# Optimization experiments

Hardware: AMD Instinct MI355X
Metric: run time of the kernel (lower is better)

The kernel has to match this reference:

```python
import jax, jax.numpy as jnp
import numpy as np

B, T, E = 2, 4096, 768
N_HEADS = 12
HEAD_DIM = E // N_HEADS


def setup_inputs() -> dict:
    key = jax.random.key(0)
    k1, k2, k3 = jax.random.split(key, 3)
    x = jax.random.normal(k1, (B, T, E), dtype=jnp.float32)
    W_attn = jax.random.normal(k2, (E, 3 * E), dtype=jnp.float32) * (1.0 / np.sqrt(E))
    b_attn = jnp.zeros((3 * E,), dtype=jnp.float32)
    W_proj = jax.random.normal(k3, (E, E), dtype=jnp.float32) * (1.0 / np.sqrt(E))
    b_proj = jnp.zeros((E,), dtype=jnp.float32)
    return {"x": x, "W_attn": W_attn, "b_attn": b_attn, "W_proj": W_proj, "b_proj": b_proj}


def reference(x, W_attn, b_attn, W_proj, b_proj):
    Bx, Tx, Ex = x.shape
    qkv = x @ W_attn + b_attn                      # [B,T,3E]
    q, k, v = jnp.split(qkv, 3, axis=-1)
    # [B,T,E] -> [B,H,T,D]
    def to_heads(t):
        return t.reshape(Bx, Tx, N_HEADS, HEAD_DIM).transpose(0, 2, 1, 3)
    q, k, v = to_heads(q), to_heads(k), to_heads(v)
    scale = 1.0 / np.sqrt(HEAD_DIM).astype(np.float32)
    scores = jnp.einsum('bhqd,bhkd->bhqk', q, k) * scale  # [B,H,T,T]
    causal = jnp.tril(jnp.ones((Tx, Tx), dtype=bool))
    scores = jnp.where(causal[None, None, :, :], scores, -jnp.inf)
    probs = jax.nn.softmax(scores, axis=-1)
    y = jnp.einsum('bhqk,bhkd->bhqd', probs, v)    # [B,H,T,D]
    y = y.transpose(0, 2, 1, 3).reshape(Bx, Tx, Ex)
    return y @ W_proj + b_proj
```

## Files before the change

kernel.cpp:

```cpp
#include <hip/hip_runtime.h>


#define SEQT 4096
#define EMB  768
#define NHEAD 12
#define HDIM 64
#define NCHUNK 144

typedef __attribute__((ext_vector_type(8))) short bf16x8;
typedef __attribute__((ext_vector_type(4))) float f32x4;
typedef __attribute__((ext_vector_type(16))) float f32x16;

static __device__ __forceinline__ unsigned short f2bf(float f) {
  union { float f; unsigned u; } a; a.f = f;
  unsigned u = a.u;
  u += 0x7FFF + ((u >> 16) & 1);
  return (unsigned short)(u >> 16);
}

static __device__ __forceinline__ unsigned pack_bf16(float a, float b) {
  union { float f; unsigned u; } ua, ub; ua.f = a; ub.f = b;
  return __builtin_amdgcn_perm(ub.u + 0x8000u, ua.u + 0x8000u, 0x07060302u);
}

static __device__ __forceinline__ void gload_lds16(const short* g, short* l) {
  __builtin_amdgcn_global_load_lds(
      (const __attribute__((address_space(1))) unsigned*)(const void*)g,
      (__attribute__((address_space(3))) unsigned*)(void*)l, 16, 0, 0);
}

__global__ __launch_bounds__(256) void cast_bf16_kernel(
    const float* __restrict__ in, short* __restrict__ out, int n4) {
  int i = blockIdx.x * 256 + threadIdx.x;
  if (i >= n4) return;
  float4 v = ((const float4*)in)[i];
  ushort4 o;
  o.x = f2bf(v.x); o.y = f2bf(v.y); o.z = f2bf(v.z); o.w = f2bf(v.w);
  ((ushort4*)out)[i] = o;
}

__global__ __launch_bounds__(256) void transpose_bf16_kernel(
    const float* __restrict__ in, short* __restrict__ out, int R, int C) {
  __shared__ float tile[32][33];
  int c0 = blockIdx.x * 32, r0 = blockIdx.y * 32;
  int tx = threadIdx.x, ty = threadIdx.y;
#pragma unroll
  for (int j = 0; j < 32; j += 8)
    tile[ty + j][tx] = in[(size_t)(r0 + ty + j) * C + (c0 + tx)];
  __syncthreads();
#pragma unroll
  for (int j = 0; j < 32; j += 8)
    out[(size_t)(c0 + ty + j) * R + (r0 + tx)] = (short)f2bf(tile[tx][ty + j]);
}

template <int MODE>
__global__ __launch_bounds__(256) void gemm128_kernel(
    const short* __restrict__ A, const short* __restrict__ Bt,
    const float* __restrict__ bias, int K,
    short* __restrict__ Qg, short* __restrict__ Kg, short* __restrict__ Vtg,
    float* __restrict__ Out) {
  __shared__ short As[128 * 32];
  __shared__ short Bs[128 * 32];
  int tid = threadIdx.x;
  int w = tid >> 6, l = tid & 63, quad = l >> 4, lo = l & 15;
  int wm = (w >> 1) * 64, wn = (w & 1) * 64;
  int gm = blockIdx.x, gn = blockIdx.y;
  f32x4 acc[4][4] = {};
  int c0 = tid, c1 = tid + 256;
  const short* Ag0 = A + (size_t)(gm * 128 + (c0 >> 2)) * K + (c0 & 3) * 8;
  const short* Ag1 = A + (size_t)(gm * 128 + (c1 >> 2)) * K + (c1 & 3) * 8;
  const short* Bg0 = Bt + (size_t)(gn * 128 + (c0 >> 2)) * K + (c0 & 3) * 8;
  const short* Bg1 = Bt + (size_t)(gn * 128 + (c1 >> 2)) * K + (c1 & 3) * 8;

  for (int kk = 0; kk < K; kk += 32) {
    gload_lds16(Ag0 + kk, &As[c0 * 8]);
    gload_lds16(Ag1 + kk, &As[c1 * 8]);
    gload_lds16(Bg0 + kk, &Bs[c0 * 8]);
    gload_lds16(Bg1 + kk, &Bs[c1 * 8]);
    __syncthreads();
    bf16x8 af[4], bf[4];
#pragma unroll
    for (int mt = 0; mt < 4; mt++)
      af[mt] = *(const bf16x8*)&As[(wm + mt * 16 + lo) * 32 + quad * 8];
#pragma unroll
    for (int nt = 0; nt < 4; nt++)
      bf[nt] = *(const bf16x8*)&Bs[(wn + nt * 16 + lo) * 32 + quad * 8];
#pragma unroll
    for (int mt = 0; mt < 4; mt++)
#pragma unroll
      for (int nt = 0; nt < 4; nt++) {
        if (MODE == 0)
          acc[mt][nt] = __builtin_amdgcn_mfma_f32_16x16x32_bf16(bf[nt], af[mt], acc[mt][nt], 0, 0, 0);
        else
          acc[mt][nt] = __builtin_amdgcn_mfma_f32_16x16x32_bf16(af[mt], bf[nt], acc[mt][nt], 0, 0, 0);
      }
    __syncthreads();
  }

  if (MODE == 0) {
#pragma unroll
    for (int nt = 0; nt < 4; nt++) {
      int nb = gn * 128 + wn + nt * 16 + quad * 4;
      float4 bv = *(const float4*)&bias[nb];
#pragma unroll
      for (int mt = 0; mt < 4; mt++) {
        int m = gm * 128 + wm + mt * 16 + lo;
        int b = m >> 12, t = m & 4095;
        float v0 = acc[mt][nt][0] + bv.x;
        float v1 = acc[mt][nt][1] + bv.y;
        float v2 = acc[mt][nt][2] + bv.z;
        float v3 = acc[mt][nt][3] + bv.w;
        if (nb < EMB) {
          int h = nb >> 6, d = nb & 63;
          uint2 u; u.x = pack_bf16(v0, v1); u.y = pack_bf16(v2, v3);
          *(uint2*)&Qg[(((size_t)b * NHEAD + h) * SEQT + t) * HDIM + d] = u;
        } else if (nb < 2 * EMB) {
          int n2 = nb - EMB, h = n2 >> 6, d = n2 & 63;
          uint2 u; u.x = pack_bf16(v0, v1); u.y = pack_bf16(v2, v3);
          *(uint2*)&Kg[(((size_t)b * NHEAD + h) * SEQT + t) * HDIM + d] = u;
        } else {
          int n2 = nb - 2 * EMB, h = n2 >> 6, d = n2 & 63;
          short* vp = &Vtg[(((size_t)b * NHEAD + h) * HDIM + d) * SEQT + t];
          vp[0] = (short)f2bf(v0);
          vp[SEQT] = (short)f2bf(v1);
          vp[2 * SEQT] = (short)f2bf(v2);
          vp[3 * SEQT] = (short)f2bf(v3);
        }
      }
    }
  } else {
#pragma unroll
    for (int nt = 0; nt < 4; nt++) {
      int n = gn * 128 + wn + nt * 16 + lo;
      float bias_v = bias[n];
#pragma unroll
      for (int mt = 0; mt < 4; mt++) {
#pragma unroll
        for (int r = 0; r < 4; r++) {
          int m = gm * 128 + wm + mt * 16 + quad * 4 + r;
          Out[(size_t)m * EMB + n] = acc[mt][nt][r] + bias_v;
        }
      }
    }
  }
}

#define AP 72
#define NEG_BIG (-1e9f)
__global__ __launch_bounds__(256, 4) void attn_kernel(
    const short* __restrict__ Qg, const short* __restrict__ Kg,
    const short* __restrict__ Vtg, short* __restrict__ Opart,
    float2* __restrict__ Ml) {
  __shared__ short Ks[64 * AP];
  __shared__ short Vs[64 * AP];
  int tid = threadIdx.x;
  int w = tid >> 6, l = tid & 63;
  int li = l & 31, hi = l >> 5;
  int c = blockIdx.x;
  int bh = blockIdx.y;
  int qt = 31, rem = c;
  while (rem >= ((qt + 4) >> 2)) { rem -= (qt + 4) >> 2; qt--; }
  int p = rem;
  int q0 = qt * 128;
  int cid = bh * NCHUNK + c;
  const short* Qbase = Qg + (size_t)bh * SEQT * HDIM;
  const short* Kbase = Kg + (size_t)bh * SEQT * HDIM;
  const short* Vbase = Vtg + (size_t)bh * HDIM * SEQT;

  int qw = q0 + w * 32;
  bf16x8 qf[4];
#pragma unroll
  for (int kk = 0; kk < 4; kk++)
    qf[kk] = *(const bf16x8*)&Qbase[(size_t)(qw + li) * HDIM + kk * 16 + hi * 8];

  f32x16 O[2] = {};
  float m_s = NEG_BIG;
  float l_s = 0.f;

  int sr = tid >> 2, sc = tid & 3;
  const float SC = 0.18033688011112042f;
  int s_begin = 8 * p;
  int s_end = min(8 * p + 8, 2 * qt + 2);

  for (int s = s_begin; s < s_end; s++) {
    int kv0 = s * 64;
    const short* kg = &Kbase[(size_t)(kv0 + sr) * HDIM + sc * 8];
    const short* vg = &Vbase[(size_t)sr * SEQT + kv0 + sc * 8];
    uint4 k0 = *(const uint4*)kg;
    uint4 k1 = *(const uint4*)(kg + 32);
    uint4 v0 = *(const uint4*)vg;
    uint4 v1 = *(const uint4*)(vg + 32);
    *(uint4*)&Ks[sr * AP + sc * 8] = k0;
    *(uint4*)&Ks[sr * AP + sc * 8 + 32] = k1;
    *(uint4*)&Vs[sr * AP + sc * 8] = v0;
    *(uint4*)&Vs[sr * AP + sc * 8 + 32] = v1;
    __syncthreads();

    if (kv0 <= qw) {
      bool act1 = (kv0 + 32 <= qw);
      bf16x8 ka0[4], ka1[4];
#pragma unroll
      for (int kk = 0; kk < 4; kk++)
        ka0[kk] = *(const bf16x8*)&Ks[li * AP + kk * 16 + hi * 8];
      if (act1) {
#pragma unroll
        for (int kk = 0; kk < 4; kk++)
          ka1[kk] = *(const bf16x8*)&Ks[(32 + li) * AP + kk * 16 + hi * 8];
      }

      f32x16 st[2];
      {
        f32x16 a = {};
#pragma unroll
        for (int kk = 0; kk < 4; kk++)
          a = __builtin_amdgcn_mfma_f32_32x32x16_bf16(ka0[kk], qf[kk], a, 0, 0, 0);
        st[0] = a;
      }
      if (act1) {
        f32x16 a = {};
#pragma unroll
        for (int kk = 0; kk < 4; kk++)
          a = __builtin_amdgcn_mfma_f32_32x32x16_bf16(ka1[kk], qf[kk], a, 0, 0, 0);
        st[1] = a;
      }

      bool full0 = (kv0 < qw);
      float mx = NEG_BIG;
      if (full0) {
#pragma unroll
        for (int r = 0; r < 16; r++) mx = fmaxf(mx, st[0][r]);
      } else {
        int thr = li - 4 * hi;
#pragma unroll
        for (int r = 0; r < 16; r++) {
          const int R = (r & 3) + 8 * (r >> 2);
          st[0][r] = (R <= thr) ? st[0][r] : NEG_BIG;
          mx = fmaxf(mx, st[0][r]);
        }
      }
      if (act1) {
        bool full1 = (kv0 + 32 < qw);
        if (full1) {
#pragma unroll
          for (int r = 0; r < 16; r++) mx = fmaxf(mx, st[1][r]);
        } else {
          int thr = li - 4 * hi;
#pragma unroll
          for (int r = 0; r < 16; r++) {
            const int R = (r & 3) + 8 * (r >> 2);
            st[1][r] = (R <= thr) ? st[1][r] : NEG_BIG;
            mx = fmaxf(mx, st[1][r]);
          }
        }
      }
      mx = fmaxf(mx, __shfl_xor(mx, 32));
      float mn = fmaxf(m_s, mx);
      float c1 = SC * mn;
      float al = __builtin_amdgcn_exp2f(fminf(SC * m_s - c1, 0.f));
      m_s = mn;
      float sm = 0.f;
      unsigned pk[2][8];
#pragma unroll
      for (int r2 = 0; r2 < 8; r2++) {
        float pa = __builtin_amdgcn_exp2f(fminf(__builtin_fmaf(st[0][2 * r2],     SC, -c1), 0.f));
        float pb = __builtin_amdgcn_exp2f(fminf(__builtin_fmaf(st[0][2 * r2 + 1], SC, -c1), 0.f));
        sm += pa + pb;
        pk[0][r2] = pack_bf16(pa, pb);
      }
      if (act1) {
#pragma unroll
        for (int r2 = 0; r2 < 8; r2++) {
          float pa = __builtin_amdgcn_exp2f(fminf(__builtin_fmaf(st[1][2 * r2],     SC, -c1), 0.f));
          float pb = __builtin_amdgcn_exp2f(fminf(__builtin_fmaf(st[1][2 * r2 + 1], SC, -c1), 0.f));
          sm += pa + pb;
          pk[1][r2] = pack_bf16(pa, pb);
        }
      }
      sm += __shfl_xor(sm, 32);
      l_s = l_s * al + sm;
#pragma unroll
      for (int dt = 0; dt < 2; dt++)
#pragma unroll
        for (int r = 0; r < 16; r++) O[dt][r] *= al;

#pragma unroll
      for (int g = 0; g < 4; g++) {
        int t = g >> 1, k2 = g & 1;
        if (t == 1 && !act1) continue;
        unsigned own_a = hi ? pk[t][k2 * 4 + 2] : pk[t][k2 * 4 + 0];
        unsigned own_b = hi ? pk[t][k2 * 4 + 3] : pk[t][k2 * 4 + 1];
        unsigned snd_a = hi ? pk[t][k2 * 4 + 0] : pk[t][k2 * 4 + 2];
        unsigned snd_b = hi ? pk[t][k2 * 4 + 1] : pk[t][k2 * 4 + 3];
        unsigned rcv_a = (unsigned)__shfl_xor((int)snd_a, 32);
        unsigned rcv_b = (unsigned)__shfl_xor((int)snd_b, 32);
        union { unsigned u[4]; bf16x8 v; } pf;
        pf.u[0] = hi ? rcv_a : own_a;
        pf.u[1] = hi ? rcv_b : own_b;
        pf.u[2] = hi ? own_a : rcv_a;
        pf.u[3] = hi ? own_b : rcv_b;
        bf16x8 va0 = *(const bf16x8*)&Vs[li * AP + g * 16 + hi * 8];
        bf16x8 va1 = *(const bf16x8*)&Vs[(32 + li) * AP + g * 16 + hi * 8];
        O[0] = __builtin_amdgcn_mfma_f32_32x32x16_bf16(va0, pf.v, O[0], 0, 0, 0);
        O[1] = __builtin_amdgcn_mfma_f32_32x32x16_bf16(va1, pf.v, O[1], 0, 0, 0);
      }
    }
    __syncthreads();
  }

  int lq = w * 32 + li;
  short* op = &Opart[((size_t)cid * 128 + lq) * 64];
#pragma unroll
  for (int dt = 0; dt < 2; dt++) {
#pragma unroll
    for (int rg = 0; rg < 4; rg++) {
      uint2 u2;
      u2.x = pack_bf16(O[dt][rg * 4 + 0], O[dt][rg * 4 + 1]);
      u2.y = pack_bf16(O[dt][rg * 4 + 2], O[dt][rg * 4 + 3]);
      *(uint2*)(op + dt * 32 + rg * 8 + hi * 4) = u2;
    }
  }
  if (hi == 0) {
    float2 ml; ml.x = m_s; ml.y = l_s;
    Ml[(size_t)cid * 128 + lq] = ml;
  }
}

__global__ __launch_bounds__(256) void merge_kernel(
    const short* __restrict__ Opart, const float2* __restrict__ Ml,
    short* __restrict__ Y) {
  int qt = blockIdx.x, bh = blockIdx.y;
  int n = (qt + 4) >> 2;
  int cbase = 0;
  for (int j = qt + 1; j < 32; j++) cbase += (j + 4) >> 2;
  int tid = threadIdx.x;
  int lq = tid >> 1, half = tid & 1;
  int b = bh / NHEAD, h = bh % NHEAD;
  int q = qt * 128 + lq;
  const float SC = 0.18033688011112042f;

  float m_i[8], l_i[8];
  float mstar = NEG_BIG;
#pragma unroll 4
  for (int i = 0; i < n; i++) {
    float2 ml = Ml[((size_t)bh * NCHUNK + cbase + i) * 128 + lq];
    m_i[i] = ml.x; l_i[i] = ml.y;
    mstar = fmaxf(mstar, ml.x);
  }
  float lstar = 0.f;
  float wgt[8];
#pragma unroll 4
  for (int i = 0; i < n; i++) {
    wgt[i] = __builtin_amdgcn_exp2f(fminf(SC * (m_i[i] - mstar), 0.f));
    lstar += l_i[i] * wgt[i];
  }

  float acc[32] = {};
#pragma unroll 4
  for (int i = 0; i < n; i++) {
    const short* op = &Opart[(((size_t)bh * NCHUNK + cbase + i) * 128 + lq) * 64 + half * 32];
    float wi = wgt[i];
#pragma unroll
    for (int v = 0; v < 4; v++) {
      uint4 u = ((const uint4*)op)[v];
      unsigned uu[4] = {u.x, u.y, u.z, u.w};
#pragma unroll
      for (int j = 0; j < 4; j++) {
        union { unsigned u; float f; } lo2, hi2;
        lo2.u = uu[j] << 16;
        hi2.u = uu[j] & 0xFFFF0000u;
        acc[v * 8 + j * 2]     = __builtin_fmaf(lo2.f, wi, acc[v * 8 + j * 2]);
        acc[v * 8 + j * 2 + 1] = __builtin_fmaf(hi2.f, wi, acc[v * 8 + j * 2 + 1]);
      }
    }
  }
  float rl = 1.f / lstar;
  short* yp = &Y[((size_t)b * SEQT + q) * EMB + h * 64 + half * 32];
#pragma unroll
  for (int v = 0; v < 4; v++) {
    uint2 u2;
    u2.x = pack_bf16(acc[v * 8 + 0] * rl, acc[v * 8 + 1] * rl);
    u2.y = pack_bf16(acc[v * 8 + 2] * rl, acc[v * 8 + 3] * rl);
    uint2 u3;
    u3.x = pack_bf16(acc[v * 8 + 4] * rl, acc[v * 8 + 5] * rl);
    u3.y = pack_bf16(acc[v * 8 + 6] * rl, acc[v * 8 + 7] * rl);
    *(uint2*)(yp + v * 8) = u2;
    *(uint2*)(yp + v * 8 + 4) = u3;
  }
}

extern "C" void kernel_launch(void* const* d_in, const int* in_sizes, int n_in,
                              void* d_out, int out_size, void* d_ws, size_t ws_size,
                              hipStream_t stream) {
  const float* x      = (const float*)d_in[0];
  const float* W_attn = (const float*)d_in[1];
  const float* b_attn = (const float*)d_in[2];
  const float* W_proj = (const float*)d_in[3];
  const float* b_proj = (const float*)d_in[4];
  float* out = (float*)d_out;

  char* ws = (char*)d_ws;
  short* x_bf  = (short*)(ws + 0);
  short* Wt_a  = (short*)(ws + 12582912);
  short* Wt_p  = (short*)(ws + 16121856);
  short* Qg    = (short*)(ws + 17301504);
  short* Kg    = (short*)(ws + 29884416);
  short* Vtg   = (short*)(ws + 42467328);
  short* Ybf   = (short*)(ws + 55050240);
  short* Opart = (short*)(ws + 67633152);
  float2* Ml   = (float2*)(ws + 124256256);

  cast_bf16_kernel<<<6144, 256, 0, stream>>>(x, x_bf, 1572864);
  transpose_bf16_kernel<<<dim3(72, 24), dim3(32, 8), 0, stream>>>(W_attn, Wt_a, 768, 2304);
  transpose_bf16_kernel<<<dim3(24, 24), dim3(32, 8), 0, stream>>>(W_proj, Wt_p, 768, 768);

  gemm128_kernel<0><<<dim3(64, 18), 256, 0, stream>>>(x_bf, Wt_a, b_attn, 768,
                                                      Qg, Kg, Vtg, nullptr);
  attn_kernel<<<dim3(NCHUNK, 24), 256, 0, stream>>>(Qg, Kg, Vtg, Opart, Ml);
  merge_kernel<<<dim3(32, 24), 256, 0, stream>>>(Opart, Ml, Ybf);
  gemm128_kernel<1><<<dim3(64, 6), 256, 0, stream>>>(Ybf, Wt_p, b_proj, 768,
                                                     nullptr, nullptr, nullptr, out);
}
```

Before: 286.6 us.

## Double-buffer K/V tiles in attention kernel with register prefetch

Splits the K/V shared-memory tiles into two buffers and issues the global loads for the next tile into registers before computing the current one, writing them into the alternate buffer afterward. This overlaps global memory latency with MFMA compute and removes one of the two barriers per iteration. In exchange it doubles LDS use per block (about 36KB), which may limit occupancy at 4 blocks per CU, and it adds register pressure from the prefetched values.

```diff
diff --git a/kernel.cpp b/kernel.cpp
--- a/kernel.cpp
+++ b/kernel.cpp
@@ -151,8 +151,8 @@
     const short* __restrict__ Qg, const short* __restrict__ Kg,
     const short* __restrict__ Vtg, short* __restrict__ Opart,
     float2* __restrict__ Ml) {
-  __shared__ short Ks[64 * AP];
-  __shared__ short Vs[64 * AP];
+  __shared__ short Ks[2][64 * AP];
+  __shared__ short Vs[2][64 * AP];
   int tid = threadIdx.x;
   int w = tid >> 6, l = tid & 63;
   int li = l & 31, hi = l >> 5;
@@ -181,31 +181,46 @@
   const float SC = 0.18033688011112042f;
   int s_begin = 8 * p;
   int s_end = min(8 * p + 8, 2 * qt + 2);
-
-  for (int s = s_begin; s < s_end; s++) {
-    int kv0 = s * 64;
+  int nsteps = s_end - s_begin;
+
+  uint4 ck0, ck1, cv0, cv1;
+  {
+    int kv0 = s_begin * 64;
     const short* kg = &Kbase[(size_t)(kv0 + sr) * HDIM + sc * 8];
     const short* vg = &Vbase[(size_t)sr * SEQT + kv0 + sc * 8];
-    uint4 k0 = *(const uint4*)kg;
-    uint4 k1 = *(const uint4*)(kg + 32);
-    uint4 v0 = *(const uint4*)vg;
-    uint4 v1 = *(const uint4*)(vg + 32);
-    *(uint4*)&Ks[sr * AP + sc * 8] = k0;
-    *(uint4*)&Ks[sr * AP + sc * 8 + 32] = k1;
-    *(uint4*)&Vs[sr * AP + sc * 8] = v0;
-    *(uint4*)&Vs[sr * AP + sc * 8 + 32] = v1;
+    ck0 = *(const uint4*)kg;  ck1 = *(const uint4*)(kg + 32);
+    cv0 = *(const uint4*)vg;  cv1 = *(const uint4*)(vg + 32);
+  }
+  *(uint4*)&Ks[0][sr * AP + sc * 8] = ck0;
+  *(uint4*)&Ks[0][sr * AP + sc * 8 + 32] = ck1;
+  *(uint4*)&Vs[0][sr * AP + sc * 8] = cv0;
+  *(uint4*)&Vs[0][sr * AP + sc * 8 + 32] = cv1;
+
+  for (int i = 0; i < nsteps; i++) {
+    int kv0 = (s_begin + i) * 64;
     __syncthreads();
+
+    if (i + 1 < nsteps) {
+      int kn = kv0 + 64;
+      const short* kg = &Kbase[(size_t)(kn + sr) * HDIM + sc * 8];
+      const short* vg = &Vbase[(size_t)sr * SEQT + kn + sc * 8];
+      ck0 = *(const uint4*)kg;  ck1 = *(const uint4*)(kg + 32);
+      cv0 = *(const uint4*)vg;  cv1 = *(const uint4*)(vg + 32);
+    }
+
+    const short* Kc = Ks[i & 1];
+    const short* Vc = Vs[i & 1];
 
     if (kv0 <= qw) {
       bool act1 = (kv0 + 32 <= qw);
       bf16x8 ka0[4], ka1[4];
 #pragma unroll
       for (int kk = 0; kk < 4; kk++)
-        ka0[kk] = *(const bf16x8*)&Ks[li * AP + kk * 16 + hi * 8];
+        ka0[kk] = *(const bf16x8*)&Kc[li * AP + kk * 16 + hi * 8];
       if (act1) {
 #pragma unroll
         for (int kk = 0; kk < 4; kk++)
-          ka1[kk] = *(const bf16x8*)&Ks[(32 + li) * AP + kk * 16 + hi * 8];
+          ka1[kk] = *(const bf16x8*)&Kc[(32 + li) * AP + kk * 16 + hi * 8];
       }
 
       f32x16 st[2];
@@ -298,13 +313,20 @@
         pf.u[1] = hi ? rcv_b : own_b;
         pf.u[2] = hi ? own_a : rcv_a;
         pf.u[3] = hi ? own_b : rcv_b;
-        bf16x8 va0 = *(const bf16x8*)&Vs[li * AP + g * 16 + hi * 8];
-        bf16x8 va1 = *(const bf16x8*)&Vs[(32 + li) * AP + g * 16 + hi * 8];
+        bf16x8 va0 = *(const bf16x8*)&Vc[li * AP + g * 16 + hi * 8];
+        bf16x8 va1 = *(const bf16x8*)&Vc[(32 + li) * AP + g * 16 + hi * 8];
         O[0] = __builtin_amdgcn_mfma_f32_32x32x16_bf16(va0, pf.v, O[0], 0, 0, 0);
         O[1] = __builtin_amdgcn_mfma_f32_32x32x16_bf16(va1, pf.v, O[1], 0, 0, 0);
       }
     }
-    __syncthreads();
+
+    if (i + 1 < nsteps) {
+      int bnext = (i + 1) & 1;
+      *(uint4*)&Ks[bnext][sr * AP + sc * 8] = ck0;
+      *(uint4*)&Ks[bnext][sr * AP + sc * 8 + 32] = ck1;
+      *(uint4*)&Vs[bnext][sr * AP + sc * 8] = cv0;
+      *(uint4*)&Vs[bnext][sr * AP + sc * 8 + 32] = cv1;
+    }
   }
 
   int lq = w * 32 + li;
```

After: 335.5 us. 1.17x slower.
